# Performance work log

Hardware: AMD Instinct MI355X
Metric: run time of the kernel (lower is better)

## Reference

```python
import jax, jax.numpy as jnp
import numpy as np

HIDDEN = 768
HEADS = 12
HEAD_DIM = HIDDEN // HEADS
LN_EPS = 1e-12


def setup_inputs() -> dict:
    key = jax.random.key(0)
    ks = jax.random.split(key, 12)
    B, Lq, Lk = 8, 512, 1024
    s = 0.02
    return {
        "query": jax.random.normal(ks[0], (B, Lq, HIDDEN), jnp.float32),
        "key": jax.random.normal(ks[1], (B, Lk, HIDDEN), jnp.float32),
        "value": jax.random.normal(ks[2], (B, Lk, HIDDEN), jnp.float32),
        "attention_mask": jnp.zeros((B, 1, 1, Lk), jnp.float32),
        "q_attention_mask": jnp.zeros((B, 1, 1, Lq), jnp.float32),
        "Wq": jax.random.normal(ks[3], (HIDDEN, HIDDEN), jnp.float32) * s,
        "bq": jnp.zeros((HIDDEN,), jnp.float32),
        "Wk": jax.random.normal(ks[4], (HIDDEN, HIDDEN), jnp.float32) * s,
        "bk": jnp.zeros((HIDDEN,), jnp.float32),
        "Wv": jax.random.normal(ks[5], (HIDDEN, HIDDEN), jnp.float32) * s,
        "bv": jnp.zeros((HIDDEN,), jnp.float32),
        "Wo": jax.random.normal(ks[6], (HIDDEN, HIDDEN), jnp.float32) * s,
        "bo": jnp.zeros((HIDDEN,), jnp.float32),
        "ln_gamma": jnp.ones((HIDDEN,), jnp.float32),
        "ln_beta": jnp.zeros((HIDDEN,), jnp.float32),
    }


def _split_heads(x):  # [B, L, H*D] -> [B, H, L, D]
    B, L, _ = x.shape
    return x.reshape(B, L, HEADS, HEAD_DIM).transpose(0, 2, 1, 3)


def reference(query, key, value, attention_mask, q_attention_mask,
              Wq, bq, Wk, bk, Wv, bv, Wo, bo, ln_gamma, ln_beta):
    # QKV projections (dropout is identity at inference)
    q = _split_heads(query @ Wq.T + bq)   # [B,H,Lq,D]
    k = _split_heads(key @ Wk.T + bk)     # [B,H,Lk,D]
    v = _split_heads(value @ Wv.T + bv)   # [B,H,Lk,D]

    scores = jnp.einsum("bhqd,bhkd->bhqk", q, k) / jnp.sqrt(
        jnp.asarray(HEAD_DIM, q.dtype))
    scores = scores + attention_mask  # additive mask broadcast [B,1,1,Lk]
    probs = jax.nn.softmax(scores, axis=-1)
    ctx = jnp.einsum("bhqk,bhkd->bhqd", probs, v)  # [B,H,Lq,D]
    B, H, Lq, D = ctx.shape
    ctx = ctx.transpose(0, 2, 1, 3).reshape(B, Lq, H * D)

    # BertSelfOutput: dense + residual + LayerNorm
    h = ctx @ Wo.T + bo + query
    mu = jnp.mean(h, axis=-1, keepdims=True)
    var = jnp.mean(jnp.square(h - mu), axis=-1, keepdims=True)
    out = (h - mu) / jnp.sqrt(var + LN_EPS) * ln_gamma + ln_beta
    return out, probs
```

## Files before the change

### kernel.cpp

```cpp
#include <hip/hip_runtime.h>
#include <math.h>

#define HIDDEN 768
#define NHEADS 12
#define DHEAD  64
#define NB     8
#define LQ     512
#define LK     1024
#define LN_EPS 1e-12f
#define TS     1032

typedef __attribute__((ext_vector_type(8))) short short8;
typedef __attribute__((ext_vector_type(4))) float floatx4;

#define GLDS16(gp, lp) __builtin_amdgcn_global_load_lds( \
    (const __attribute__((address_space(1))) void*)(gp), \
    (__attribute__((address_space(3))) void*)(lp), 16, 0, 0)

__device__ __forceinline__ short f2bf(float f) {
    unsigned u = __float_as_uint(f);
    u = u + 0x7FFFu + ((u >> 16) & 1u);
    return (short)(u >> 16);
}

__device__ __forceinline__ float bf2f(short s) {
    return __uint_as_float(((unsigned)(unsigned short)s) << 16);
}

__global__ __launch_bounds__(256)
void cvt_all(const float* __restrict__ q, const float* __restrict__ k,
             const float* __restrict__ v,
             const float* __restrict__ Wq, const float* __restrict__ Wk,
             const float* __restrict__ Wv, const float* __restrict__ Wo,
             short* __restrict__ dq, short* __restrict__ dk,
             short* __restrict__ dv,
             short* __restrict__ dwq, short* __restrict__ dwk,
             short* __restrict__ dwv, short* __restrict__ dwo)
{
    int bx = blockIdx.x;
    const float* src; short* dst; int base;
    if (bx < 3072)       { src = q; dst = dq; base = bx; }
    else if (bx < 9216)  { src = k; dst = dk; base = bx - 3072; }
    else if (bx < 15360) { src = v; dst = dv; base = bx - 9216; }
    else {
        int wb = bx - 15360, wsel = wb / 576;
        base = wb - wsel * 576;
        src = (wsel == 0) ? Wq : (wsel == 1) ? Wk : (wsel == 2) ? Wv : Wo;
        dst = (wsel == 0) ? dwq : (wsel == 1) ? dwk : (wsel == 2) ? dwv : dwo;
    }
    int i = base * 256 + threadIdx.x;
    float4 vv = ((const float4*)src)[i];
    short4 o;
    o.x = f2bf(vv.x); o.y = f2bf(vv.y); o.z = f2bf(vv.z); o.w = f2bf(vv.w);
    ((short4*)dst)[i] = o;
}

__device__ __forceinline__ void gemm_core(
    short (*As)[4096], short (*Bs)[4096],
    const short* __restrict__ A, const short* __restrict__ B,
    float* Cf, short* Cb,
    const float* bias, const float* res,
    int m0, int n0, int K, int lda, int ldb, int ldc, float alpha)
{
    int t    = threadIdx.x;
    int lane = t & 63, wave = t >> 6;
    int quad = lane >> 4, l15 = lane & 15;
    int wr = wave >> 1, wc = wave & 1;

    int e0 = t, e1 = 256 + t;
    int r0 = e0 >> 2, c0 = (e0 & 3) ^ ((r0 >> 1) & 3);
    int r1 = e1 >> 2, c1 = (e1 & 3) ^ ((r1 >> 1) & 3);
    const short* Ap0 = A + (size_t)(m0 + r0) * lda + c0 * 8;
    const short* Ap1 = A + (size_t)(m0 + r1) * lda + c1 * 8;
    const short* Bp0 = B + (size_t)(n0 + r0) * ldb + c0 * 8;
    const short* Bp1 = B + (size_t)(n0 + r1) * ldb + c1 * 8;

    int aoff[4], boff[4];
#pragma unroll
    for (int i = 0; i < 4; i++) {
        int ra = wr * 64 + i * 16 + l15;
        aoff[i] = (ra * 4 + (quad ^ ((ra >> 1) & 3))) * 8;
        int rb = wc * 64 + i * 16 + l15;
        boff[i] = (rb * 4 + (quad ^ ((rb >> 1) & 3))) * 8;
    }

    floatx4 acc[4][4] = {};
    int nsteps = K >> 5;

    GLDS16(Ap0, &As[0][e0 * 8]);
    GLDS16(Ap1, &As[0][e1 * 8]);
    GLDS16(Bp0, &Bs[0][e0 * 8]);
    GLDS16(Bp1, &Bs[0][e1 * 8]);
    Ap0 += 32; Ap1 += 32; Bp0 += 32; Bp1 += 32;

    for (int s = 0; s < nsteps; s++) {
        int cur = s & 1;
        __syncthreads();
        if (s + 1 < nsteps) {
            GLDS16(Ap0, &As[cur ^ 1][e0 * 8]);
            GLDS16(Ap1, &As[cur ^ 1][e1 * 8]);
            GLDS16(Bp0, &Bs[cur ^ 1][e0 * 8]);
            GLDS16(Bp1, &Bs[cur ^ 1][e1 * 8]);
            Ap0 += 32; Ap1 += 32; Bp0 += 32; Bp1 += 32;
        }
        short8 af[4], bfr[4];
#pragma unroll
        for (int i = 0; i < 4; i++) af[i]  = *(const short8*)&As[cur][aoff[i]];
#pragma unroll
        for (int j = 0; j < 4; j++) bfr[j] = *(const short8*)&Bs[cur][boff[j]];
#pragma unroll
        for (int i = 0; i < 4; i++)
#pragma unroll
            for (int j = 0; j < 4; j++)
                acc[i][j] = __builtin_amdgcn_mfma_f32_16x16x32_bf16(
                    af[i], bfr[j], acc[i][j], 0, 0, 0);
    }

#pragma unroll
    for (int i = 0; i < 4; i++) {
        int mb = m0 + wr * 64 + i * 16 + quad * 4;
#pragma unroll
        for (int j = 0; j < 4; j++) {
            int n = n0 + wc * 64 + j * 16 + l15;
            float bv = bias ? bias[n] : 0.f;
#pragma unroll
            for (int r = 0; r < 4; r++) {
                int m = mb + r;
                float v = alpha * acc[i][j][r] + bv;
                if (res) v += res[(size_t)m * ldc + n];
                if (Cb) Cb[(size_t)m * ldc + n] = f2bf(v);
                else    Cf[(size_t)m * ldc + n] = v;
            }
        }
    }
}

__global__ __launch_bounds__(256)
void gemm_nt_mfma(const short* __restrict__ A, const short* __restrict__ B,
                  float* __restrict__ Cf, short* __restrict__ Cb,
                  const float* __restrict__ bias, const float* __restrict__ res,
                  int K, int lda, int ldb, int ldc, float alpha)
{
    __shared__ short As[2][4096];
    __shared__ short Bs[2][4096];
    gemm_core(As, Bs, A, B, Cf, Cb, bias, res,
              blockIdx.y * 128, blockIdx.x * 128, K, lda, ldb, ldc, alpha);
}

__global__ __launch_bounds__(256)
void qkv_gemm(const short* __restrict__ qx, const short* __restrict__ kx,
              const short* __restrict__ vx,
              const short* __restrict__ wq, const short* __restrict__ wk,
              const short* __restrict__ wv,
              const float* __restrict__ bq, const float* __restrict__ bk,
              const float* __restrict__ bv,
              short* __restrict__ qb, short* __restrict__ kb,
              short* __restrict__ vb)
{
    __shared__ short As[2][4096];
    __shared__ short Bs[2][4096];
    int yb = blockIdx.y;
    const short *A, *B; const float* bias; short* C; int m0;
    if (yb < 32)      { A = qx; B = wq; bias = bq; C = qb; m0 = yb * 128; }
    else if (yb < 96) { A = kx; B = wk; bias = bk; C = kb; m0 = (yb - 32) * 128; }
    else              { A = vx; B = wv; bias = bv; C = vb; m0 = (yb - 96) * 128; }
    gemm_core(As, Bs, A, B, nullptr, C, bias, nullptr,
              m0, blockIdx.x * 128, HIDDEN, HIDDEN, HIDDEN, HIDDEN, 1.0f);
}

__global__ __launch_bounds__(256)
void transpose_v(const short* __restrict__ vb, short* __restrict__ vt)
{
    __shared__ short T[256 * 72];
    int kt = blockIdx.x, bh = blockIdx.y;
    int b = bh / 12, h = bh - b * 12;
    int t = threadIdx.x;
    const short* src = vb + ((size_t)b * LK + kt * 256) * HIDDEN + h * DHEAD;
#pragma unroll
    for (int it = 0; it < 8; it++) {
        int s = it * 256 + t;
        int k = s >> 3, c = s & 7;
        *(short8*)&T[k * 72 + c * 8] =
            *(const short8*)&src[(size_t)k * HIDDEN + c * 8];
    }
    __syncthreads();
    short* dst = vt + (size_t)bh * DHEAD * LK + kt * 256;
#pragma unroll
    for (int it = 0; it < 8; it++) {
        int s = it * 256 + t;
        int d = s >> 5, kc = s & 31;
        short8 v;
#pragma unroll
        for (int i = 0; i < 8; i++) v[i] = T[(kc * 8 + i) * 72 + d];
        *(short8*)&dst[(size_t)d * LK + kc * 8] = v;
    }
}

__global__ __launch_bounds__(256)
void fused_attn(const short* __restrict__ qb, const short* __restrict__ kb,
                const short* __restrict__ vt, const float* __restrict__ amask,
                float* __restrict__ probs, short* __restrict__ ctxb)
{
    __shared__ short S[16 * TS];
    __shared__ short KV[8192];
    __shared__ float mpart[4][16];
    __shared__ float lrow[16];

    int flat = blockIdx.y * 32 + blockIdx.x;
    int jj   = flat >> 3;
    int bh   = (flat & 7) * 12 + jj % 12;
    int qt   = jj / 12;
    int b = bh / 12, h = bh - b * 12;
    int m0 = qt * 16;

    const short* Qg = qb + ((size_t)b * LQ + m0) * HIDDEN + h * DHEAD;
    const short* Kg = kb + (size_t)b * LK * HIDDEN + h * DHEAD;
    const short* Vg = vt + (size_t)bh * DHEAD * LK;
    const float* Mg = amask + (size_t)b * LK;
    float* Pg = probs + (size_t)bh * LQ * LK + (size_t)m0 * LK;
    short* Cg = ctxb + ((size_t)b * LQ + m0) * HIDDEN + h * DHEAD;

    int t = threadIdx.x;
    int lane = t & 63, w = t >> 6;
    int quad = lane >> 4, l15 = lane & 15;

#pragma unroll
    for (int I = 0; I < 4; I++) {
        int s = I * 256 + t;
        int r = s >> 3, cs = s & 7, c = cs ^ (r & 7);
        GLDS16(Kg + (size_t)r * HIDDEN + c * 8, &KV[s * 8]);
    }

    short8 af[2];
#pragma unroll
    for (int ks = 0; ks < 2; ks++)
        af[ks] = *(const short8*)&Qg[(size_t)l15 * HIDDEN + ks * 32 + quad * 8];

    float mx[4];
#pragma unroll
    for (int r = 0; r < 4; r++) mx[r] = -3.0e38f;

    const float SC  = 0.125f * 1.44269504089f;
    const float L2E = 1.44269504089f;

    for (int kc = 0; kc < 8; kc++) {
        __syncthreads();
        floatx4 acc[2] = {};
#pragma unroll
        for (int ks = 0; ks < 2; ks++)
#pragma unroll
            for (int j = 0; j < 2; j++) {
                int rK = w * 32 + j * 16 + l15;
                int cs = (ks * 4 + quad) ^ (rK & 7);
                short8 bfr = *(const short8*)&KV[(rK * 8 + cs) * 8];
                acc[j] = __builtin_amdgcn_mfma_f32_16x16x32_bf16(
                    af[ks], bfr, acc[j], 0, 0, 0);
            }
        __syncthreads();
        if (kc < 7) {
            const short* Kn = Kg + (size_t)(kc + 1) * 128 * HIDDEN;
#pragma unroll
            for (int I = 0; I < 4; I++) {
                int s = I * 256 + t;
                int r = s >> 3, cs = s & 7, c = cs ^ (r & 7);
                GLDS16(Kn + (size_t)r * HIDDEN + c * 8, &KV[s * 8]);
            }
        }
#pragma unroll
        for (int j = 0; j < 2; j++) {
            int n = kc * 128 + w * 32 + j * 16 + l15;
            float mk = Mg[n] * L2E;
#pragma unroll
            for (int r = 0; r < 4; r++) {
                int m = quad * 4 + r;
                float v = acc[j][r] * SC + mk;
                S[m * TS + n] = f2bf(v);
                mx[r] = fmaxf(mx[r], v);
            }
        }
    }

#pragma unroll
    for (int d = 1; d < 16; d <<= 1)
#pragma unroll
        for (int r = 0; r < 4; r++)
            mx[r] = fmaxf(mx[r], __shfl_xor(mx[r], d));
    if (l15 == 0)
#pragma unroll
        for (int r = 0; r < 4; r++)
            mpart[w][quad * 4 + r] = mx[r];
    __syncthreads();

#pragma unroll
    for (int I = 0; I < 4; I++) {
        int s = I * 256 + t;
        int n = s >> 4, cs = s & 15, c = cs ^ (n & 15);
        GLDS16(Vg + (size_t)n * LK + c * 8, &KV[s * 8]);
    }

    {
        int r = t >> 4, seg = t & 15;
        float mr = fmaxf(fmaxf(mpart[0][r], mpart[1][r]),
                         fmaxf(mpart[2][r], mpart[3][r]));
        float sum = 0.f;
#pragma unroll
        for (int i = 0; i < 8; i++) {
            int u = i * 16 + seg;
            short8 v = *(const short8*)&S[r * TS + u * 8];
            short8 o;
#pragma unroll
            for (int e = 0; e < 8; e++) {
                float f = exp2f(bf2f(v[e]) - mr);
                o[e] = f2bf(f);
                sum += f;
            }
            *(short8*)&S[r * TS + u * 8] = o;
        }
        sum += __shfl_xor(sum, 1);
        sum += __shfl_xor(sum, 2);
        sum += __shfl_xor(sum, 4);
        sum += __shfl_xor(sum, 8);
        if (seg == 0) lrow[r] = sum;
    }

    floatx4 accO = {};
    for (int kc = 0; kc < 8; kc++) {
        __syncthreads();
#pragma unroll
        for (int ks = 0; ks < 4; ks++) {
            short8 pa = *(const short8*)&S[l15 * TS + kc * 128
                                           + ks * 32 + quad * 8];
            int n = w * 16 + l15;
            int cs = (ks * 4 + quad) ^ (n & 15);
            short8 bfr = *(const short8*)&KV[(n * 16 + cs) * 8];
            accO = __builtin_amdgcn_mfma_f32_16x16x32_bf16(
                pa, bfr, accO, 0, 0, 0);
        }
        __syncthreads();
        if (kc < 7) {
            const short* Vn = Vg + (kc + 1) * 128;
#pragma unroll
            for (int I = 0; I < 4; I++) {
                int s = I * 256 + t;
                int n = s >> 4, cs = s & 15, c = cs ^ (n & 15);
                GLDS16(Vn + (size_t)n * LK + c * 8, &KV[s * 8]);
            }
        }
#pragma unroll
        for (int rr = 0; rr < 2; rr++) {
            int r = kc * 2 + rr;
            float inv = 1.0f / lrow[r];
            short4 v = *(const short4*)&S[r * TS + t * 4];
            floatx4 o;
            o.x = bf2f(v.x) * inv; o.y = bf2f(v.y) * inv;
            o.z = bf2f(v.z) * inv; o.w = bf2f(v.w) * inv;
            __builtin_nontemporal_store(
                o, (floatx4*)(Pg + (size_t)r * LK) + t);
        }
    }

    int n = w * 16 + l15;
#pragma unroll
    for (int r = 0; r < 4; r++) {
        int m = quad * 4 + r;
        Cg[(size_t)m * HIDDEN + n] = f2bf(accO[r] / lrow[m]);
    }
}

__global__ __launch_bounds__(256)
void layernorm_rows(const float* __restrict__ H, const float* __restrict__ gamma,
                    const float* __restrict__ beta, float* __restrict__ out)
{
    int row = blockIdx.x;
    const float* h = H + (long)row * HIDDEN;
    int t = threadIdx.x;

    float x[3];
    float s = 0.f, ss = 0.f;
#pragma unroll
    for (int i = 0; i < 3; i++) {
        x[i] = h[t + 256 * i];
        s  += x[i];
        ss += x[i] * x[i];
    }
#pragma unroll
    for (int off = 32; off > 0; off >>= 1) {
        s  += __shfl_down(s, off);
        ss += __shfl_down(ss, off);
    }
    __shared__ float sh_s[4], sh_ss[4];
    int wave = t >> 6;
    if ((t & 63) == 0) { sh_s[wave] = s; sh_ss[wave] = ss; }
    __syncthreads();
    float S  = sh_s[0] + sh_s[1] + sh_s[2] + sh_s[3];
    float SS = sh_ss[0] + sh_ss[1] + sh_ss[2] + sh_ss[3];

    float mu  = S * (1.0f / HIDDEN);
    float var = SS * (1.0f / HIDDEN) - mu * mu;
    float inv = rsqrtf(var + LN_EPS);

    float* o = out + (long)row * HIDDEN;
#pragma unroll
    for (int i = 0; i < 3; i++) {
        int c = t + 256 * i;
        o[c] = (x[i] - mu) * inv * gamma[c] + beta[c];
    }
}

extern "C" void kernel_launch(void* const* d_in, const int* in_sizes, int n_in,
                              void* d_out, int out_size, void* d_ws, size_t ws_size,
                              hipStream_t stream)
{
    const float* query = (const float*)d_in[0];
    const float* key   = (const float*)d_in[1];
    const float* value = (const float*)d_in[2];
    const float* amask = (const float*)d_in[3];
    const float* Wq    = (const float*)d_in[5];
    const float* bq    = (const float*)d_in[6];
    const float* Wk    = (const float*)d_in[7];
    const float* bk    = (const float*)d_in[8];
    const float* Wv    = (const float*)d_in[9];
    const float* bv    = (const float*)d_in[10];
    const float* Wo    = (const float*)d_in[11];
    const float* bo    = (const float*)d_in[12];
    const float* gamma = (const float*)d_in[13];
    const float* beta  = (const float*)d_in[14];

    short* qx = (short*)d_ws;
    short* kx = qx + (long)4096 * 768;
    short* vx = kx + (long)8192 * 768;
    short* wq = vx + (long)8192 * 768;
    short* wk = wq + (long)768 * 768;
    short* wv = wk + (long)768 * 768;
    short* wo = wv + (long)768 * 768;
    short* qb = wo + (long)768 * 768;
    short* kb = qb + (long)4096 * 768;
    short* vb = kb + (long)8192 * 768;
    short* ctxb = qx;
    short* vt   = kx;
    float* hbuf = (float*)vx;

    float* out0  = (float*)d_out;
    float* probs = out0 + (long)NB * LQ * HIDDEN;

    cvt_all<<<17664, 256, 0, stream>>>(query, key, value, Wq, Wk, Wv, Wo,
                                       qx, kx, vx, wq, wk, wv, wo);

    qkv_gemm<<<dim3(6, 160), 256, 0, stream>>>(
        qx, kx, vx, wq, wk, wv, bq, bk, bv, qb, kb, vb);

    transpose_v<<<dim3(4, 96), 256, 0, stream>>>(vb, vt);

    fused_attn<<<dim3(32, 96), 256, 0, stream>>>(qb, kb, vt, amask, probs, ctxb);

    gemm_nt_mfma<<<dim3(6, 32), 256, 0, stream>>>(
        ctxb, wo, hbuf, nullptr, bo, query, HIDDEN, HIDDEN, HIDDEN, HIDDEN, 1.0f);

    layernorm_rows<<<NB * LQ, 256, 0, stream>>>(hbuf, gamma, beta, out0);
}
```

Before: 436.4 us.

## Replace direct global-to-LDS loads with register-staged K/V prefetch two chunks ahead

Drops the global_load_lds DMA for K and V tiles in the attention kernel. Each tile is now loaded into registers two iterations ahead and written to LDS after the compute barrier, which moves the next chunk's global latency off the critical path. The sync points are reshuffled to match. This costs extra VGPRs for the staging buffers plus explicit LDS write instructions, which could lower occupancy.

New measurement: 437.3 us. About the same (+0.2%).

```diff
diff --git a/kernel.cpp b/kernel.cpp
--- a/kernel.cpp
+++ b/kernel.cpp
@@ -224,17 +224,43 @@
     int lane = t & 63, w = t >> 6;
     int quad = lane >> 4, l15 = lane & 15;
 
+    short8 stg[4];
+
+    int sK_r[4], sK_c[4], sV_n[4], sV_c[4];
 #pragma unroll
     for (int I = 0; I < 4; I++) {
         int s = I * 256 + t;
-        int r = s >> 3, cs = s & 7, c = cs ^ (r & 7);
-        GLDS16(Kg + (size_t)r * HIDDEN + c * 8, &KV[s * 8]);
-    }
-
+        int r = s >> 3, cs = s & 7;
+        sK_r[I] = r; sK_c[I] = (cs ^ (r & 7)) * 8;
+        int n = s >> 4, cv = s & 15;
+        sV_n[I] = n; sV_c[I] = (cv ^ (n & 15)) * 8;
+    }
+
+#define LOAD_K(kc) { \
+    const short* Kn = Kg + (size_t)(kc) * 128 * HIDDEN; \
+    _Pragma("unroll") \
+    for (int I = 0; I < 4; I++) \
+        stg[I] = *(const short8*)&Kn[(size_t)sK_r[I] * HIDDEN + sK_c[I]]; }
+
+#define LOAD_V(kc) { \
+    const short* Vn = Vg + (kc) * 128; \
+    _Pragma("unroll") \
+    for (int I = 0; I < 4; I++) \
+        stg[I] = *(const short8*)&Vn[(size_t)sV_n[I] * LK + sV_c[I]]; }
+
+#define WRITE_KV() { \
+    _Pragma("unroll") \
+    for (int I = 0; I < 4; I++) \
+        *(short8*)&KV[(I * 256 + t) * 8] = stg[I]; }
+
+    LOAD_K(0);
     short8 af[2];
 #pragma unroll
     for (int ks = 0; ks < 2; ks++)
         af[ks] = *(const short8*)&Qg[(size_t)l15 * HIDDEN + ks * 32 + quad * 8];
+    WRITE_KV();
+    LOAD_K(1);
+    __syncthreads();
 
     float mx[4];
 #pragma unroll
@@ -244,7 +270,6 @@
     const float L2E = 1.44269504089f;
 
     for (int kc = 0; kc < 8; kc++) {
-        __syncthreads();
         floatx4 acc[2] = {};
 #pragma unroll
         for (int ks = 0; ks < 2; ks++)
@@ -258,13 +283,9 @@
             }
         __syncthreads();
         if (kc < 7) {
-            const short* Kn = Kg + (size_t)(kc + 1) * 128 * HIDDEN;
-#pragma unroll
-            for (int I = 0; I < 4; I++) {
-                int s = I * 256 + t;
-                int r = s >> 3, cs = s & 7, c = cs ^ (r & 7);
-                GLDS16(Kn + (size_t)r * HIDDEN + c * 8, &KV[s * 8]);
-            }
+            WRITE_KV();
+            if (kc < 6) { LOAD_K(kc + 2); }
+            else        { LOAD_V(0); }
         }
 #pragma unroll
         for (int j = 0; j < 2; j++) {
@@ -278,6 +299,7 @@
                 mx[r] = fmaxf(mx[r], v);
             }
         }
+        __syncthreads();
     }
 
 #pragma unroll
@@ -291,12 +313,8 @@
             mpart[w][quad * 4 + r] = mx[r];
     __syncthreads();
 
-#pragma unroll
-    for (int I = 0; I < 4; I++) {
-        int s = I * 256 + t;
-        int n = s >> 4, cs = s & 15, c = cs ^ (n & 15);
-        GLDS16(Vg + (size_t)n * LK + c * 8, &KV[s * 8]);
-    }
+    WRITE_KV();
+    LOAD_V(1);
 
     {
         int r = t >> 4, seg = t & 15;
@@ -322,10 +340,10 @@
         sum += __shfl_xor(sum, 8);
         if (seg == 0) lrow[r] = sum;
     }
+    __syncthreads();
 
     floatx4 accO = {};
     for (int kc = 0; kc < 8; kc++) {
-        __syncthreads();
 #pragma unroll
         for (int ks = 0; ks < 4; ks++) {
             short8 pa = *(const short8*)&S[l15 * TS + kc * 128
@@ -338,13 +356,8 @@
         }
         __syncthreads();
         if (kc < 7) {
-            const short* Vn = Vg + (kc + 1) * 128;
-#pragma unroll
-            for (int I = 0; I < 4; I++) {
-                int s = I * 256 + t;
-                int n = s >> 4, cs = s & 15, c = cs ^ (n & 15);
-                GLDS16(Vn + (size_t)n * LK + c * 8, &KV[s * 8]);
-            }
+            WRITE_KV();
+            if (kc < 6) { LOAD_V(kc + 2); }
         }
 #pragma unroll
         for (int rr = 0; rr < 2; rr++) {
@@ -357,6 +370,7 @@
             __builtin_nontemporal_store(
                 o, (floatx4*)(Pg + (size_t)r * LK) + t);
         }
+        __syncthreads();
     }
 
     int n = w * 16 + l15;
@@ -365,6 +379,9 @@
         int m = quad * 4 + r;
         Cg[(size_t)m * HIDDEN + n] = f2bf(accO[r] / lrow[m]);
     }
+#undef LOAD_K
+#undef LOAD_V
+#undef WRITE_KV
 }
 
 __global__ __launch_bounds__(256)
```
